# Kernel optimization log

Hardware: AMD Instinct MI355X
Metric: run time of the kernel (lower is better)

## Reference

```python
import jax, jax.numpy as jnp
import numpy as np

B, T, I, H, O = 64, 512, 64, 1024, 64
STEPS = 49 - 1  # output_len - 1 decode iterations


def _cell(x_t, h, c, Wih, Whh, b):
    # PyTorch LSTM gate order: i, f, g, o
    gates = x_t @ Wih.T + h @ Whh.T + b  # [B, 4H]
    i, f, g, o = jnp.split(gates, 4, axis=-1)
    i = jax.nn.sigmoid(i)
    f = jax.nn.sigmoid(f)
    g = jnp.tanh(g)
    o = jax.nn.sigmoid(o)
    c2 = f * c + i * g
    h2 = o * jnp.tanh(c2)
    return h2, c2


def setup_inputs() -> dict:
    key = jax.random.key(0)
    ks = jax.random.split(key, 12)
    s = 0.05
    return {
        "x": jax.random.normal(ks[0], (B, T, I), jnp.float32),
        "y0": jax.random.normal(ks[1], (B, I), jnp.float32),
        "Wih_e": jax.random.normal(ks[2], (4 * H, I), jnp.float32) * s,
        "Whh_e": jax.random.normal(ks[3], (4 * H, H), jnp.float32) * s,
        "bih_e": jax.random.normal(ks[4], (4 * H,), jnp.float32) * s,
        "bhh_e": jax.random.normal(ks[5], (4 * H,), jnp.float32) * s,
        "Wih_d": jax.random.normal(ks[6], (4 * H, I), jnp.float32) * s,
        "Whh_d": jax.random.normal(ks[7], (4 * H, H), jnp.float32) * s,
        "bih_d": jax.random.normal(ks[8], (4 * H,), jnp.float32) * s,
        "bhh_d": jax.random.normal(ks[9], (4 * H,), jnp.float32) * s,
        "Wfc": jax.random.normal(ks[10], (O, H), jnp.float32) * s,
        "bfc": jax.random.normal(ks[11], (O,), jnp.float32) * s,
    }


def reference(x, y0, Wih_e, Whh_e, bih_e, bhh_e, Wih_d, Whh_d, bih_d, bhh_d, Wfc, bfc):
    b = x.shape[0]
    h0 = jnp.zeros((b, Whh_e.shape[1]), x.dtype)
    c0 = h0

    # Encoder: scan over time (zero initial hidden, as in initHidden)
    be = bih_e + bhh_e

    def enc_step(carry, x_t):
        h, c = carry
        h, c = _cell(x_t, h, c, Wih_e, Whh_e, be)
        return (h, c), None

    (h, c), _ = jax.lax.scan(enc_step, (h0, c0), jnp.swapaxes(x, 0, 1))

    # Decoder: original loop never updates input_decoder -> constant y0 each step.
    bd = bih_d + bhh_d
    xin = y0 @ Wih_d.T + bd  # precompute constant input projection [B, 4H]

    def dec_step(carry, _):
        hd, cd = carry
        gates = xin + hd @ Whh_d.T
        i, f, g, o = jnp.split(gates, 4, axis=-1)
        i = jax.nn.sigmoid(i)
        f = jax.nn.sigmoid(f)
        g = jnp.tanh(g)
        o = jax.nn.sigmoid(o)
        c2 = f * cd + i * g
        h2 = o * jnp.tanh(c2)
        out = h2 @ Wfc.T + bfc  # [B, O]
        return (h2, c2), out

    _, ys = jax.lax.scan(dec_step, (h, c), None, length=STEPS)  # [STEPS, B, O]
    # torch.concat(total, dim=1): step-major along feature axis
    return jnp.swapaxes(ys, 0, 1).reshape(b, STEPS * ys.shape[-1])
```

## Files before the change

### kernel.cpp

```cpp
#include <hip/hip_runtime.h>
#include <hip/hip_fp16.h>

typedef _Float16 f16;
typedef _Float16 f16x8 __attribute__((ext_vector_type(8)));
typedef float f32x16 __attribute__((ext_vector_type(16)));

#define T_N 512
#define DSTEPS 48
#define TOTSTEPS 560
#define NWG 64

#define OFF_WHHE 0ull
#define SZ_WHH   (4096ull*1024*2)
#define OFF_WHHD (OFF_WHHE + SZ_WHH)
#define OFF_WIHE (OFF_WHHD + SZ_WHH)
#define SZ_WIH   (4096ull*64*2)
#define OFF_WIHD (OFF_WIHE + SZ_WIH)
#define OFF_WFC  (OFF_WIHD + SZ_WIH)
#define SZ_WFC   (64ull*1024*2)
#define OFF_XP   (OFF_WFC + SZ_WFC)
#define SZ_XP    (512ull*4096*2)
#define OFF_Y0   (OFF_XP + SZ_XP)
#define SZ_Y0    (4096ull*2)
#define OFF_BE   (OFF_Y0 + SZ_Y0)
#define OFF_BD   (OFF_BE + 4096ull*4)
#define OFF_FLG  (OFF_BD + 4096ull*4)
#define SZ_FLG   (561ull*256*4)
#define OFF_H    ((OFF_FLG + SZ_FLG + 255ull) & ~255ull)

__global__ void prologue(const float* __restrict__ x, const float* __restrict__ y0,
    const float* __restrict__ wihE, const float* __restrict__ whhE,
    const float* __restrict__ bihE, const float* __restrict__ bhhE,
    const float* __restrict__ wihD, const float* __restrict__ whhD,
    const float* __restrict__ bihD, const float* __restrict__ bhhD,
    const float* __restrict__ wfc, char* __restrict__ ws)
{
  const long long gid = (long long)blockIdx.x * 256 + threadIdx.x;
  const long long gsz = (long long)gridDim.x * 256;
  f16* whhEp = (f16*)(ws + OFF_WHHE);
  f16* whhDp = (f16*)(ws + OFF_WHHD);
  f16* wihEp = (f16*)(ws + OFF_WIHE);
  f16* wihDp = (f16*)(ws + OFF_WIHD);
  f16* wfcp  = (f16*)(ws + OFF_WFC);
  f16* xp    = (f16*)(ws + OFF_XP);
  f16* y0p   = (f16*)(ws + OFF_Y0);
  float* be  = (float*)(ws + OFF_BE);
  float* bd  = (float*)(ws + OFF_BD);

  for (long long idx = gid; idx < 4194304ll; idx += gsz) {
    int j = (int)idx & 7, l = (int)(idx >> 3) & 63, kk = (int)(idx >> 9) & 31;
    int i = (int)(idx >> 14) & 1, ks = (int)(idx >> 15) & 1, w = (int)(idx >> 16);
    int nl = i * 32 + (l & 31);
    int grow = (nl >> 4) * 1024 + w * 16 + (nl & 15);
    int k = ks * 512 + kk * 16 + ((l >> 5) << 3) + j;
    whhEp[idx] = (f16)whhE[(long long)grow * 1024 + k];
    whhDp[idx] = (f16)whhD[(long long)grow * 1024 + k];
  }
  for (long long idx = gid; idx < 262144ll; idx += gsz) {
    int j = (int)idx & 7, l = (int)(idx >> 3) & 63, kx = (int)(idx >> 9) & 1;
    int i = (int)(idx >> 10) & 1, ks = (int)(idx >> 11) & 1, w = (int)(idx >> 12);
    int nl = i * 32 + (l & 31);
    int grow = (nl >> 4) * 1024 + w * 16 + (nl & 15);
    int k = (ks * 2 + kx) * 16 + ((l >> 5) << 3) + j;
    wihEp[idx] = (f16)wihE[grow * 64 + k];
    wihDp[idx] = (f16)wihD[grow * 64 + k];
  }
  for (long long idx = gid; idx < 65536ll; idx += gsz) {
    int j = (int)idx & 7, l = (int)(idx >> 3) & 63, kk = (int)(idx >> 9) & 31;
    int i = (int)(idx >> 14) & 1, ks = (int)(idx >> 15) & 1;
    int o = i * 32 + (l & 31);
    int k = ks * 512 + kk * 16 + ((l >> 5) << 3) + j;
    wfcp[idx] = (f16)wfc[o * 1024 + k];
  }
  for (long long idx = gid; idx < 2097152ll; idx += gsz) {
    int kw = (int)idx & 15, b = (int)(idx >> 4) & 63, kkx = (int)(idx >> 10) & 3, t = (int)(idx >> 12);
    xp[idx] = (f16)x[(long long)b * 32768 + t * 64 + kkx * 16 + kw];
  }
  for (long long idx = gid; idx < 4096ll; idx += gsz) {
    int kw = (int)idx & 15, b = (int)(idx >> 4) & 63, kkx = (int)(idx >> 10) & 3;
    y0p[idx] = (f16)y0[b * 64 + kkx * 16 + kw];
  }
  for (long long idx = gid; idx < 4096ll; idx += gsz) {
    be[idx] = bihE[idx] + bhhE[idx];
    bd[idx] = bihD[idx] + bhhD[idx];
  }
}

__device__ __forceinline__ float sigf(float x) { return 1.0f / (1.0f + __expf(-x)); }
__device__ __forceinline__ float tanhfast(float x) {
  x = fminf(fmaxf(x, -15.f), 15.f);
  float e = __expf(2.0f * x);
  return (e - 1.0f) / (e + 1.0f);
}

#define MFMA(a,b,c) __builtin_amdgcn_mfma_f32_32x32x16_f16((a),(b),(c),0,0,0)

__launch_bounds__(256, 1)
__global__ void lstm_persist(char* __restrict__ ws, float* __restrict__ out,
                             const float* __restrict__ bfc)
{
  const int w    = blockIdx.x;
  const int tid  = threadIdx.x;
  const int lane = tid & 63;
  const int wave = tid >> 6;
  const int wm   = wave & 1;
  const int ks   = wave >> 1;

  const f16* whhEp = (const f16*)(ws + OFF_WHHE) + (size_t)w * 65536;
  const f16* whhDp = (const f16*)(ws + OFF_WHHD) + (size_t)w * 65536;
  const f16* wihEp = (const f16*)(ws + OFF_WIHE) + (size_t)w * 4096;
  const f16* wihDp = (const f16*)(ws + OFF_WIHD) + (size_t)w * 4096;
  const f16* wfcp  = (const f16*)(ws + OFF_WFC);
  const f16* xp    = (const f16*)(ws + OFF_XP);
  const f16* y0p   = (const f16*)(ws + OFF_Y0);
  const float* be  = (const float*)(ws + OFF_BE);
  const float* bd  = (const float*)(ws + OFF_BD);
  unsigned* flags  = (unsigned*)(ws + OFF_FLG);
  f16* hb          = (f16*)(ws + OFF_H);

  __shared__ float lds_g[2][64][66];
  __shared__ float bias_s[2][64];

  if (tid < 64) {
    int g4 = tid >> 4, u = tid & 15;
    bias_s[0][tid] = be[g4 * 1024 + w * 16 + u];
    bias_s[1][tid] = bd[g4 * 1024 + w * 16 + u];
  }

  const int aoff = (wm * 32 + (lane & 31)) * 16 + (lane >> 5) * 8;
  const int boff = lane * 8;
  const int bsel = tid >> 2;
  const int u0   = (tid & 3) * 4;

  f16x8 bf0[32], bf1[32];
#pragma unroll
  for (int kk = 0; kk < 32; ++kk) {
    bf0[kk] = *(const f16x8*)(whhEp + (size_t)ks * 32768 + kk * 512 + boff);
    bf1[kk] = *(const f16x8*)(whhEp + (size_t)ks * 32768 + 16384 + kk * 512 + boff);
  }

  float c0 = 0.f, c1 = 0.f, c2 = 0.f, c3 = 0.f;
  __syncthreads();

#pragma unroll 1
  for (int t = 0; t < TOTSTEPS; ++t) {
    const bool enc = (t < T_N);

    if (t == T_N) {
#pragma unroll
      for (int kk = 0; kk < 32; ++kk) {
        bf0[kk] = *(const f16x8*)(whhDp + (size_t)ks * 32768 + kk * 512 + boff);
        bf1[kk] = *(const f16x8*)(whhDp + (size_t)ks * 32768 + 16384 + kk * 512 + boff);
      }
    }

    const f16* xblk = enc ? (xp + (size_t)t * 4096) : y0p;
    const f16* wihp = enc ? wihEp : wihDp;
    f16x8 xa0 = *(const f16x8*)(xblk + (ks * 2 + 0) * 1024 + aoff);
    f16x8 xa1 = *(const f16x8*)(xblk + (ks * 2 + 1) * 1024 + aoff);
    f16x8 wf0 = *(const f16x8*)(wihp + ((ks * 2 + 0) * 2 + 0) * 512 + boff);
    f16x8 wf1 = *(const f16x8*)(wihp + ((ks * 2 + 0) * 2 + 1) * 512 + boff);
    f16x8 wf2 = *(const f16x8*)(wihp + ((ks * 2 + 1) * 2 + 0) * 512 + boff);
    f16x8 wf3 = *(const f16x8*)(wihp + ((ks * 2 + 1) * 2 + 1) * 512 + boff);

    if (t > 0) {
      const unsigned* fp0 = flags + (size_t)t * 256 + lane;
      int ok;
      do {
        unsigned v0 = __hip_atomic_load(fp0,       __ATOMIC_RELAXED, __HIP_MEMORY_SCOPE_AGENT);
        unsigned v1 = __hip_atomic_load(fp0 + 64,  __ATOMIC_RELAXED, __HIP_MEMORY_SCOPE_AGENT);
        unsigned v2 = __hip_atomic_load(fp0 + 128, __ATOMIC_RELAXED, __HIP_MEMORY_SCOPE_AGENT);
        unsigned v3 = __hip_atomic_load(fp0 + 192, __ATOMIC_RELAXED, __HIP_MEMORY_SCOPE_AGENT);
        ok = (v0 == 1u) & (v1 == 1u) & (v2 == 1u) & (v3 == 1u);
      } while (__syncthreads_and(ok) == 0);
    }

    f16x8 af[32];
    if (t > 0) {
      const f16* hblk = hb + (size_t)(t - 1) * 65536;
#pragma unroll
      for (int kk = 0; kk < 32; ++kk)
        af[kk] = *(const f16x8*)(hblk + (size_t)(ks * 32 + kk) * 1024 + aoff);
    }

    f32x16 acc0, acc1;
#pragma unroll
    for (int i = 0; i < 16; ++i) { acc0[i] = 0.f; acc1[i] = 0.f; }
    acc0 = MFMA(xa0, wf0, acc0); acc0 = MFMA(xa1, wf1, acc0);
    acc1 = MFMA(xa0, wf2, acc1); acc1 = MFMA(xa1, wf3, acc1);

    if (t > 0) {
#pragma unroll
      for (int kk = 0; kk < 32; ++kk) {
        acc0 = MFMA(af[kk], bf0[kk], acc0);
        acc1 = MFMA(af[kk], bf1[kk], acc1);
      }
    }

    {
      const int n0 = lane & 31;
      const int mb = wm * 32 + ((lane >> 5) << 2);
#pragma unroll
      for (int r = 0; r < 16; ++r) {
        const int m = mb + (r & 3) + ((r >> 2) << 3);
        lds_g[ks][n0][m]      = acc0[r];
        lds_g[ks][32 + n0][m] = acc1[r];
      }
    }
    __syncthreads();

    const float* bs = enc ? bias_s[0] : bias_s[1];
    union { unsigned long long u64; f16 h4[4]; } hu;
    float cc[4] = {c0, c1, c2, c3};
#pragma unroll
    for (int j = 0; j < 4; ++j) {
      const int u = u0 + j;
      float ig = lds_g[0][u][bsel]      + lds_g[1][u][bsel]      + bs[u];
      float fg = lds_g[0][16 + u][bsel] + lds_g[1][16 + u][bsel] + bs[16 + u];
      float gg = lds_g[0][32 + u][bsel] + lds_g[1][32 + u][bsel] + bs[32 + u];
      float og = lds_g[0][48 + u][bsel] + lds_g[1][48 + u][bsel] + bs[48 + u];
      float cn = sigf(fg) * cc[j] + sigf(ig) * tanhfast(gg);
      cc[j] = cn;
      hu.h4[j] = (f16)(sigf(og) * tanhfast(cn));
    }
    c0 = cc[0]; c1 = cc[1]; c2 = cc[2]; c3 = cc[3];

    {
      f16* dst = hb + (size_t)t * 65536 + (size_t)w * 1024 + bsel * 16 + u0;
      unsigned long long addr = (unsigned long long)(size_t)dst;
      asm volatile("global_store_dwordx2 %0, %1, off sc0 sc1" : : "v"(addr), "v"(hu.u64) : "memory");
    }
    asm volatile("s_waitcnt vmcnt(0)" ::: "memory");
    if (lane == 0) {
      unsigned* fa = flags + (size_t)(t + 1) * 256 + wave * 64 + w;
      unsigned long long addr = (unsigned long long)(size_t)fa;
      unsigned one = 1u;
      asm volatile("global_store_dword %0, %1, off sc0 sc1" : : "v"(addr), "v"(one) : "memory");
    }
  }

  if (w < DSTEPS) {
    const int s = T_N + 1 + w;
#pragma unroll
    for (int kk = 0; kk < 32; ++kk) {
      bf0[kk] = *(const f16x8*)(wfcp + (size_t)ks * 32768 + kk * 512 + boff);
      bf1[kk] = *(const f16x8*)(wfcp + (size_t)ks * 32768 + 16384 + kk * 512 + boff);
    }
    {
      const unsigned* fp0 = flags + (size_t)s * 256 + lane;
      int ok;
      do {
        unsigned v0 = __hip_atomic_load(fp0,       __ATOMIC_RELAXED, __HIP_MEMORY_SCOPE_AGENT);
        unsigned v1 = __hip_atomic_load(fp0 + 64,  __ATOMIC_RELAXED, __HIP_MEMORY_SCOPE_AGENT);
        unsigned v2 = __hip_atomic_load(fp0 + 128, __ATOMIC_RELAXED, __HIP_MEMORY_SCOPE_AGENT);
        unsigned v3 = __hip_atomic_load(fp0 + 192, __ATOMIC_RELAXED, __HIP_MEMORY_SCOPE_AGENT);
        ok = (v0 == 1u) & (v1 == 1u) & (v2 == 1u) & (v3 == 1u);
      } while (__syncthreads_and(ok) == 0);
    }
    const f16* hblk = hb + (size_t)(s - 1) * 65536;
    f16x8 af[32];
#pragma unroll
    for (int kk = 0; kk < 32; ++kk)
      af[kk] = *(const f16x8*)(hblk + (size_t)(ks * 32 + kk) * 1024 + aoff);

    f32x16 acc0, acc1;
#pragma unroll
    for (int i = 0; i < 16; ++i) { acc0[i] = 0.f; acc1[i] = 0.f; }
#pragma unroll
    for (int kk = 0; kk < 32; ++kk) {
      acc0 = MFMA(af[kk], bf0[kk], acc0);
      acc1 = MFMA(af[kk], bf1[kk], acc1);
    }
    {
      const int n0 = lane & 31;
      const int mb = wm * 32 + ((lane >> 5) << 2);
#pragma unroll
      for (int r = 0; r < 16; ++r) {
        const int m = mb + (r & 3) + ((r >> 2) << 3);
        lds_g[ks][n0][m]      = acc0[r];
        lds_g[ks][32 + n0][m] = acc1[r];
      }
    }
    __syncthreads();
    const int f0 = (tid & 3) * 16;
    float* op = out + (size_t)bsel * 3072 + w * 64 + f0;
#pragma unroll
    for (int c4 = 0; c4 < 4; ++c4) {
      float v4[4];
#pragma unroll
      for (int j = 0; j < 4; ++j) {
        const int f = f0 + c4 * 4 + j;
        v4[j] = lds_g[0][f][bsel] + lds_g[1][f][bsel] + bfc[f];
      }
      *(float4*)(op + c4 * 4) = make_float4(v4[0], v4[1], v4[2], v4[3]);
    }
  }
}

extern "C" void kernel_launch(void* const* d_in, const int* in_sizes, int n_in,
                              void* d_out, int out_size, void* d_ws, size_t ws_size,
                              hipStream_t stream) {
  const float* x    = (const float*)d_in[0];
  const float* y0   = (const float*)d_in[1];
  const float* wihE = (const float*)d_in[2];
  const float* whhE = (const float*)d_in[3];
  const float* bihE = (const float*)d_in[4];
  const float* bhhE = (const float*)d_in[5];
  const float* wihD = (const float*)d_in[6];
  const float* whhD = (const float*)d_in[7];
  const float* bihD = (const float*)d_in[8];
  const float* bhhD = (const float*)d_in[9];
  const float* wfc  = (const float*)d_in[10];
  const float* bfc  = (const float*)d_in[11];
  char* ws   = (char*)d_ws;
  float* out = (float*)d_out;

  prologue<<<256, 256, 0, stream>>>(x, y0, wihE, whhE, bihE, bhhE,
                                    wihD, whhD, bihD, bhhD, wfc, ws);
  lstm_persist<<<NWG, 256, 0, stream>>>(ws, out, bfc);
}
```

Baseline: 3.327 ms.

## Stage recurrent weights in LDS and poll packed byte flags from one wave

Moves the per-workgroup Whh slice from registers into a 128 KB dynamic LDS buffer, which frees the 64 f16x8 B-fragment registers at the cost of LDS reads inside the MFMA loop. The inter-workgroup flags shrink from dwords to bytes, so one wave polls a single dword per lane with s_sleep backoff and releases the other waves through an LDS token instead of a block-wide __syncthreads_and. Gate partial sums from the two k-split waves are merged with LDS atomicAdd into one buffer that is re-zeroed after being read, and biases are held in registers. Together these aim to cut per-step synchronisation latency on the serial recurrence, but LDS atomics and weight loads from LDS add latency on each step.

Measured after the change: 10.99 ms. 230% more time.

```diff
diff --git a/kernel.cpp b/kernel.cpp
--- a/kernel.cpp
+++ b/kernel.cpp
@@ -25,8 +25,10 @@
 #define OFF_BE   (OFF_Y0 + SZ_Y0)
 #define OFF_BD   (OFF_BE + 4096ull*4)
 #define OFF_FLG  (OFF_BD + 4096ull*4)
-#define SZ_FLG   (561ull*256*4)
+#define SZ_FLG   (561ull*256)
 #define OFF_H    ((OFF_FLG + SZ_FLG + 255ull) & ~255ull)
+
+#define LDS_BYTES 148224
 
 __global__ void prologue(const float* __restrict__ x, const float* __restrict__ y0,
     const float* __restrict__ wihE, const float* __restrict__ whhE,
@@ -94,6 +96,7 @@
 }
 
 #define MFMA(a,b,c) __builtin_amdgcn_mfma_f32_32x32x16_f16((a),(b),(c),0,0,0)
+#define LG(n,m) lds_g[(n)*66 + (m)]
 
 __launch_bounds__(256, 1)
 __global__ void lstm_persist(char* __restrict__ ws, float* __restrict__ out,
@@ -115,29 +118,32 @@
   const f16* y0p   = (const f16*)(ws + OFF_Y0);
   const float* be  = (const float*)(ws + OFF_BE);
   const float* bd  = (const float*)(ws + OFF_BD);
-  unsigned* flags  = (unsigned*)(ws + OFF_FLG);
+  unsigned char* flags = (unsigned char*)(ws + OFF_FLG);
   f16* hb          = (f16*)(ws + OFF_H);
 
-  __shared__ float lds_g[2][64][66];
-  __shared__ float bias_s[2][64];
-
-  if (tid < 64) {
-    int g4 = tid >> 4, u = tid & 15;
-    bias_s[0][tid] = be[g4 * 1024 + w * 16 + u];
-    bias_s[1][tid] = bd[g4 * 1024 + w * 16 + u];
-  }
+  extern __shared__ char smem[];
+  f16*   whh_lds = (f16*)smem;
+  float* lds_g   = (float*)(smem + 131072);
+  int*   tok     = (int*)(smem + 131072 + 16896);
 
   const int aoff = (wm * 32 + (lane & 31)) * 16 + (lane >> 5) * 8;
   const int boff = lane * 8;
   const int bsel = tid >> 2;
   const int u0   = (tid & 3) * 4;
 
-  f16x8 bf0[32], bf1[32];
-#pragma unroll
-  for (int kk = 0; kk < 32; ++kk) {
-    bf0[kk] = *(const f16x8*)(whhEp + (size_t)ks * 32768 + kk * 512 + boff);
-    bf1[kk] = *(const f16x8*)(whhEp + (size_t)ks * 32768 + 16384 + kk * 512 + boff);
-  }
+  float bE[16], bD[16];
+#pragma unroll
+  for (int g4 = 0; g4 < 4; ++g4)
+#pragma unroll
+    for (int j = 0; j < 4; ++j) {
+      bE[g4 * 4 + j] = be[g4 * 1024 + w * 16 + u0 + j];
+      bD[g4 * 4 + j] = bd[g4 * 1024 + w * 16 + u0 + j];
+    }
+
+  for (int i = tid; i < 8192; i += 256)
+    *(f16x8*)(whh_lds + (size_t)i * 8) = *(const f16x8*)(whhEp + (size_t)i * 8);
+  for (int i = tid; i < 64 * 66; i += 256) lds_g[i] = 0.f;
+  if (tid == 0) *tok = 0;
 
   float c0 = 0.f, c1 = 0.f, c2 = 0.f, c3 = 0.f;
   __syncthreads();
@@ -147,11 +153,10 @@
     const bool enc = (t < T_N);
 
     if (t == T_N) {
-#pragma unroll
-      for (int kk = 0; kk < 32; ++kk) {
-        bf0[kk] = *(const f16x8*)(whhDp + (size_t)ks * 32768 + kk * 512 + boff);
-        bf1[kk] = *(const f16x8*)(whhDp + (size_t)ks * 32768 + 16384 + kk * 512 + boff);
-      }
+      __syncthreads();
+      for (int i = tid; i < 8192; i += 256)
+        *(f16x8*)(whh_lds + (size_t)i * 8) = *(const f16x8*)(whhDp + (size_t)i * 8);
+      __syncthreads();
     }
 
     const f16* xblk = enc ? (xp + (size_t)t * 4096) : y0p;
@@ -163,26 +168,6 @@
     f16x8 wf2 = *(const f16x8*)(wihp + ((ks * 2 + 1) * 2 + 0) * 512 + boff);
     f16x8 wf3 = *(const f16x8*)(wihp + ((ks * 2 + 1) * 2 + 1) * 512 + boff);
 
-    if (t > 0) {
-      const unsigned* fp0 = flags + (size_t)t * 256 + lane;
-      int ok;
-      do {
-        unsigned v0 = __hip_atomic_load(fp0,       __ATOMIC_RELAXED, __HIP_MEMORY_SCOPE_AGENT);
-        unsigned v1 = __hip_atomic_load(fp0 + 64,  __ATOMIC_RELAXED, __HIP_MEMORY_SCOPE_AGENT);
-        unsigned v2 = __hip_atomic_load(fp0 + 128, __ATOMIC_RELAXED, __HIP_MEMORY_SCOPE_AGENT);
-        unsigned v3 = __hip_atomic_load(fp0 + 192, __ATOMIC_RELAXED, __HIP_MEMORY_SCOPE_AGENT);
-        ok = (v0 == 1u) & (v1 == 1u) & (v2 == 1u) & (v3 == 1u);
-      } while (__syncthreads_and(ok) == 0);
-    }
-
-    f16x8 af[32];
-    if (t > 0) {
-      const f16* hblk = hb + (size_t)(t - 1) * 65536;
-#pragma unroll
-      for (int kk = 0; kk < 32; ++kk)
-        af[kk] = *(const f16x8*)(hblk + (size_t)(ks * 32 + kk) * 1024 + aoff);
-    }
-
     f32x16 acc0, acc1;
 #pragma unroll
     for (int i = 0; i < 16; ++i) { acc0[i] = 0.f; acc1[i] = 0.f; }
@@ -190,10 +175,30 @@
     acc1 = MFMA(xa0, wf2, acc1); acc1 = MFMA(xa1, wf3, acc1);
 
     if (t > 0) {
+      if (wave == 3) {
+        const unsigned* fl = (const unsigned*)(flags + (size_t)t * 256);
+        unsigned v;
+        for (;;) {
+          v = __hip_atomic_load(fl + lane, __ATOMIC_RELAXED, __HIP_MEMORY_SCOPE_AGENT);
+          if (__all(v == 0x01010101u)) break;
+          __builtin_amdgcn_s_sleep(1);
+        }
+        __hip_atomic_store(tok, t, __ATOMIC_RELEASE, __HIP_MEMORY_SCOPE_WORKGROUP);
+      } else {
+        while (__hip_atomic_load(tok, __ATOMIC_ACQUIRE, __HIP_MEMORY_SCOPE_WORKGROUP) < t) {}
+      }
+
+      const f16* hblk = hb + (size_t)(t - 1) * 65536;
+      f16x8 af[32];
+#pragma unroll
+      for (int kk = 0; kk < 32; ++kk)
+        af[kk] = *(const f16x8*)(hblk + (size_t)(ks * 32 + kk) * 1024 + aoff);
 #pragma unroll
       for (int kk = 0; kk < 32; ++kk) {
-        acc0 = MFMA(af[kk], bf0[kk], acc0);
-        acc1 = MFMA(af[kk], bf1[kk], acc1);
+        f16x8 b0 = *(const f16x8*)(whh_lds + (size_t)ks * 32768 + kk * 512 + boff);
+        f16x8 b1 = *(const f16x8*)(whh_lds + (size_t)ks * 32768 + 16384 + kk * 512 + boff);
+        acc0 = MFMA(af[kk], b0, acc0);
+        acc1 = MFMA(af[kk], b1, acc1);
       }
     }
 
@@ -203,22 +208,22 @@
 #pragma unroll
       for (int r = 0; r < 16; ++r) {
         const int m = mb + (r & 3) + ((r >> 2) << 3);
-        lds_g[ks][n0][m]      = acc0[r];
-        lds_g[ks][32 + n0][m] = acc1[r];
+        atomicAdd(&LG(n0, m), acc0[r]);
+        atomicAdd(&LG(32 + n0, m), acc1[r]);
       }
     }
     __syncthreads();
 
-    const float* bs = enc ? bias_s[0] : bias_s[1];
     union { unsigned long long u64; f16 h4[4]; } hu;
     float cc[4] = {c0, c1, c2, c3};
 #pragma unroll
     for (int j = 0; j < 4; ++j) {
       const int u = u0 + j;
-      float ig = lds_g[0][u][bsel]      + lds_g[1][u][bsel]      + bs[u];
-      float fg = lds_g[0][16 + u][bsel] + lds_g[1][16 + u][bsel] + bs[16 + u];
-      float gg = lds_g[0][32 + u][bsel] + lds_g[1][32 + u][bsel] + bs[32 + u];
-      float og = lds_g[0][48 + u][bsel] + lds_g[1][48 + u][bsel] + bs[48 + u];
+      float ig = LG(u, bsel)      + (enc ? bE[j]      : bD[j]);
+      float fg = LG(16 + u, bsel) + (enc ? bE[4 + j]  : bD[4 + j]);
+      float gg = LG(32 + u, bsel) + (enc ? bE[8 + j]  : bD[8 + j]);
+      float og = LG(48 + u, bsel) + (enc ? bE[12 + j] : bD[12 + j]);
+      LG(u, bsel) = 0.f; LG(16 + u, bsel) = 0.f; LG(32 + u, bsel) = 0.f; LG(48 + u, bsel) = 0.f;
       float cn = sigf(fg) * cc[j] + sigf(ig) * tanhfast(gg);
       cc[j] = cn;
       hu.h4[j] = (f16)(sigf(og) * tanhfast(cn));
@@ -230,31 +235,29 @@
       unsigned long long addr = (unsigned long long)(size_t)dst;
       asm volatile("global_store_dwordx2 %0, %1, off sc0 sc1" : : "v"(addr), "v"(hu.u64) : "memory");
     }
-    asm volatile("s_waitcnt vmcnt(0)" ::: "memory");
+    asm volatile("s_waitcnt vmcnt(0) lgkmcnt(0)" ::: "memory");
     if (lane == 0) {
-      unsigned* fa = flags + (size_t)(t + 1) * 256 + wave * 64 + w;
-      unsigned long long addr = (unsigned long long)(size_t)fa;
+      unsigned long long fa = (unsigned long long)(size_t)(flags + (size_t)(t + 1) * 256 + w * 4 + wave);
       unsigned one = 1u;
-      asm volatile("global_store_dword %0, %1, off sc0 sc1" : : "v"(addr), "v"(one) : "memory");
+      asm volatile("global_store_byte %0, %1, off sc0 sc1" : : "v"(fa), "v"(one) : "memory");
     }
   }
 
   if (w < DSTEPS) {
+    __syncthreads();
     const int s = T_N + 1 + w;
+    f16x8 bf0[32], bf1[32];
 #pragma unroll
     for (int kk = 0; kk < 32; ++kk) {
       bf0[kk] = *(const f16x8*)(wfcp + (size_t)ks * 32768 + kk * 512 + boff);
       bf1[kk] = *(const f16x8*)(wfcp + (size_t)ks * 32768 + 16384 + kk * 512 + boff);
     }
     {
-      const unsigned* fp0 = flags + (size_t)s * 256 + lane;
+      const unsigned* fl = (const unsigned*)(flags + (size_t)s * 256);
       int ok;
       do {
-        unsigned v0 = __hip_atomic_load(fp0,       __ATOMIC_RELAXED, __HIP_MEMORY_SCOPE_AGENT);
-        unsigned v1 = __hip_atomic_load(fp0 + 64,  __ATOMIC_RELAXED, __HIP_MEMORY_SCOPE_AGENT);
-        unsigned v2 = __hip_atomic_load(fp0 + 128, __ATOMIC_RELAXED, __HIP_MEMORY_SCOPE_AGENT);
-        unsigned v3 = __hip_atomic_load(fp0 + 192, __ATOMIC_RELAXED, __HIP_MEMORY_SCOPE_AGENT);
-        ok = (v0 == 1u) & (v1 == 1u) & (v2 == 1u) & (v3 == 1u);
+        unsigned v = __hip_atomic_load(fl + lane, __ATOMIC_RELAXED, __HIP_MEMORY_SCOPE_AGENT);
+        ok = (v == 0x01010101u);
       } while (__syncthreads_and(ok) == 0);
     }
     const f16* hblk = hb + (size_t)(s - 1) * 65536;
@@ -277,8 +280,8 @@
 #pragma unroll
       for (int r = 0; r < 16; ++r) {
         const int m = mb + (r & 3) + ((r >> 2) << 3);
-        lds_g[ks][n0][m]      = acc0[r];
-        lds_g[ks][32 + n0][m] = acc1[r];
+        atomicAdd(&LG(n0, m), acc0[r]);
+        atomicAdd(&LG(32 + n0, m), acc1[r]);
       }
     }
     __syncthreads();
@@ -290,7 +293,7 @@
 #pragma unroll
       for (int j = 0; j < 4; ++j) {
         const int f = f0 + c4 * 4 + j;
-        v4[j] = lds_g[0][f][bsel] + lds_g[1][f][bsel] + bfc[f];
+        v4[j] = LG(f, bsel) + bfc[f];
       }
       *(float4*)(op + c4 * 4) = make_float4(v4[0], v4[1], v4[2], v4[3]);
     }
@@ -315,7 +318,10 @@
   char* ws   = (char*)d_ws;
   float* out = (float*)d_out;
 
+  (void)hipFuncSetAttribute((const void*)lstm_persist,
+                            hipFuncAttributeMaxDynamicSharedMemorySize, LDS_BYTES);
+
   prologue<<<256, 256, 0, stream>>>(x, y0, wihE, whhE, bihE, bhhE,
                                     wihD, whhD, bihD, bhhD, wfc, ws);
-  lstm_persist<<<NWG, 256, 0, stream>>>(ws, out, bfc);
+  lstm_persist<<<NWG, 256, LDS_BYTES, stream>>>(ws, out, bfc);
 }
```
